# Kernel optimization log

Measured on AMD Instinct MI355X. Metric: run time of the kernel, lower is better.

The kernel has to match this reference:

```python
import jax, jax.numpy as jnp
import numpy as np

N = 100000        # nodes
E = 1600000       # edges (avg degree 16)
F_IN = 512        # num_features
H1, D1 = 8, 8     # layer-1 heads x per-head dim (concat -> 64)
C = 16            # num_classes (layer-2: 1 head, dim C)
NEG_SLOPE = 0.2


def setup_inputs() -> dict:
    key = jax.random.key(0)
    ks = jax.random.split(key, 8)
    x = jax.random.normal(ks[0], (N, F_IN), dtype=jnp.float32)
    edge_index = jax.random.randint(ks[1], (2, E), 0, N, dtype=jnp.int64)
    W1 = jax.random.normal(ks[2], (F_IN, H1 * D1), dtype=jnp.float32) / np.float32(np.sqrt(F_IN))
    a1_src = jax.random.normal(ks[3], (H1, D1), dtype=jnp.float32) * 0.1
    a1_dst = jax.random.normal(ks[4], (H1, D1), dtype=jnp.float32) * 0.1
    W2 = jax.random.normal(ks[5], (H1 * D1, C), dtype=jnp.float32) / np.float32(np.sqrt(H1 * D1))
    a2_src = jax.random.normal(ks[6], (1, C), dtype=jnp.float32) * 0.1
    a2_dst = jax.random.normal(ks[7], (1, C), dtype=jnp.float32) * 0.1
    return {"x": x, "edge_index": edge_index, "W1": W1, "a1_src": a1_src,
            "a1_dst": a1_dst, "W2": W2, "a2_src": a2_src, "a2_dst": a2_dst}


def gat_layer(x, src, dst, W, a_s, a_d, heads, out_dim):
    """Multi-head GAT conv: gather -> per-edge leaky-relu score -> segment
    softmax over destination -> scatter-aggregate. Returns [N, heads, out_dim]."""
    n = x.shape[0]
    h = (x @ W).reshape(n, heads, out_dim)            # [N, H, D]
    es = jnp.einsum('nhd,hd->nh', h, a_s)             # source attention term
    ed = jnp.einsum('nhd,hd->nh', h, a_d)             # dest attention term
    e = jax.nn.leaky_relu(es[src] + ed[dst], NEG_SLOPE)   # [E, H]
    m = jax.ops.segment_max(e, dst, num_segments=n)       # stable softmax max
    ex = jnp.exp(e - m[dst])
    s = jax.ops.segment_sum(ex, dst, num_segments=n)
    alpha = ex / s[dst]                               # [E, H]
    out = jax.ops.segment_sum(h[src] * alpha[..., None], dst, num_segments=n)
    return out                                        # [N, H, D]


def reference(x, edge_index, W1, a1_src, a1_dst, W2, a2_src, a2_dst):
    n = x.shape[0]
    loop = jnp.arange(n, dtype=edge_index.dtype)
    src = jnp.concatenate([edge_index[0], loop])      # add self-loops
    dst = jnp.concatenate([edge_index[1], loop])
    # eval mode: dropout(p=0.6, training=False) is identity
    h1 = gat_layer(x, src, dst, W1, a1_src, a1_dst, H1, D1).reshape(n, H1 * D1)
    h1 = jax.nn.elu(h1)
    h2 = gat_layer(h1, src, dst, W2, a2_src, a2_dst, 1, C).reshape(n, C)
    return jax.nn.log_softmax(h2, axis=1)
```

## Files before the change

kernel.cpp:

```cpp
#include <hip/hip_runtime.h>
#include <hip/hip_bf16.h>

#define F_IN 512
#define H1 8
#define D1 8
#define F_MID 64
#define C 16
#define NEG_SLOPE 0.2f
#define BIN_CHUNK 4096
#define NB_MAX 1024
#define BUCKET_SHIFT 7
#define BUCKET_STRIDE 3072
#define SRC_BITS 17
#define SRC_MASK ((1 << SRC_BITS) - 1)

typedef __attribute__((ext_vector_type(8))) short bf16x8;
typedef __attribute__((ext_vector_type(4))) float f32x4;

static __device__ __forceinline__ unsigned short f2bf(float f) {
    __hip_bfloat16 h = __float2bfloat16(f);
    return *(unsigned short*)&h;
}

__global__ __launch_bounds__(256) void k_bin_w1t(const int* __restrict__ src,
                                                 const int* __restrict__ dst,
                                                 int* __restrict__ gcur,
                                                 int* __restrict__ bucketed,
                                                 const float* __restrict__ W1,
                                                 __hip_bfloat16* __restrict__ w1t,
                                                 int n_edges, int nb, int nbin) {
    const int t = threadIdx.x;
    if ((int)blockIdx.x >= nbin) {
        int idx = ((int)blockIdx.x - nbin) * 256 + t;
        int k = idx >> 6, n = idx & 63;
        w1t[n * F_IN + k] = __float2bfloat16(W1[idx]);
        return;
    }
    __shared__ int cnt[NB_MAX];
    __shared__ int base[NB_MAX];
    const int eb = blockIdx.x * BIN_CHUNK;
    int dc[BIN_CHUNK / 256];
#pragma unroll
    for (int i = 0; i < BIN_CHUNK / 256; ++i) {
        int e = eb + i * 256 + t;
        dc[i] = (e < n_edges) ? dst[e] : -1;
    }
    for (int b = t; b < nb; b += 256) cnt[b] = 0;
    __syncthreads();
#pragma unroll
    for (int i = 0; i < BIN_CHUNK / 256; ++i)
        if (dc[i] >= 0) atomicAdd(&cnt[dc[i] >> BUCKET_SHIFT], 1);
    __syncthreads();
    for (int b = t; b < nb; b += 256) {
        int c = cnt[b];
        base[b] = c > 0 ? atomicAdd(&gcur[b], c) : 0;
        cnt[b] = 0;
    }
    __syncthreads();
#pragma unroll
    for (int i = 0; i < BIN_CHUNK / 256; ++i) {
        if (dc[i] >= 0) {
            int e = eb + i * 256 + t;
            int d = dc[i];
            int b = d >> BUCKET_SHIFT;
            int local = atomicAdd(&cnt[b], 1);
            bucketed[(size_t)b * BUCKET_STRIDE + base[b] + local] =
                ((d & ((1 << BUCKET_SHIFT) - 1)) << SRC_BITS) | src[e];
        }
    }
}

__global__ __launch_bounds__(256) void k_place(const int* __restrict__ gcur,
                                               const int* __restrict__ bucketed,
                                               int* __restrict__ row_start,
                                               int* __restrict__ sorted_src,
                                               int n_nodes, int n_edges) {
    __shared__ int stage[BUCKET_STRIDE];
    __shared__ int cnt[1 << BUCKET_SHIFT];
    __shared__ int cur[1 << BUCKET_SHIFT];
    __shared__ int wsum[4];
    const int t = threadIdx.x;
    const int b = blockIdx.x;
    if (t < (1 << BUCKET_SHIFT)) cnt[t] = 0;
    int pre = 0;
    for (int j = t; j < b; j += 256) pre += gcur[j];
#pragma unroll
    for (int off = 1; off < 64; off <<= 1) pre += __shfl_xor(pre, off, 64);
    if ((t & 63) == 0) wsum[t >> 6] = pre;
    __syncthreads();
    const int base0 = wsum[0] + wsum[1] + wsum[2] + wsum[3];
    if (b == 0 && t == 0) row_start[n_nodes] = n_edges;

    const int total = gcur[b];
    const int* bp = bucketed + (size_t)b * BUCKET_STRIDE;
    for (int i = t; i < total; i += 256) {
        int e = bp[i];
        stage[i] = e;
        atomicAdd(&cnt[e >> SRC_BITS], 1);
    }
    __syncthreads();
    if (t < (1 << BUCKET_SHIFT)) cur[t] = cnt[t];
    __syncthreads();
#pragma unroll
    for (int d = 1; d < (1 << BUCKET_SHIFT); d <<= 1) {
        int u = 0;
        if (t < (1 << BUCKET_SHIFT) && t >= d) u = cur[t - d];
        __syncthreads();
        if (t < (1 << BUCKET_SHIFT)) cur[t] += u;
        __syncthreads();
    }
    if (t < (1 << BUCKET_SHIFT)) {
        int node = (b << BUCKET_SHIFT) + t;
        int excl = cur[t] - cnt[t];
        if (node < n_nodes) row_start[node] = base0 + excl;
        cur[t] = excl;
    }
    __syncthreads();
    for (int i = t; i < total; i += 256) {
        int e = stage[i];
        int p = atomicAdd(&cur[e >> SRC_BITS], 1);
        sorted_src[base0 + p] = e & SRC_MASK;
    }
}

__global__ __launch_bounds__(256) void k_gemm1(const float* __restrict__ x,
                                               const __hip_bfloat16* __restrict__ w1t,
                                               const float* __restrict__ a1s,
                                               const float* __restrict__ a1d,
                                               __hip_bfloat16* __restrict__ h1b,
                                               float* __restrict__ es1,
                                               float* __restrict__ ed1, int n_nodes) {
    const int t = threadIdx.x;
    const int wv = t >> 6, l = t & 63;
    const int q = l >> 4, m16 = l & 15;
    const int rowbase = blockIdx.x * 64;

    const int node = rowbase + wv * 16 + m16;
    const int gx = node < n_nodes ? node : n_nodes - 1;
    const float* xrow = x + (size_t)gx * F_IN;

    f32x4 acc[4];
#pragma unroll
    for (int i = 0; i < 4; ++i) acc[i] = (f32x4){0.f, 0.f, 0.f, 0.f};

    for (int kt = 0; kt < F_IN; kt += 64) {
#pragma unroll
        for (int kk = 0; kk < 2; ++kk) {
            const float* xp = xrow + kt + kk * 32 + q * 8;
            float4 v0 = *(const float4*)(xp);
            float4 v1 = *(const float4*)(xp + 4);
            ushort4 b0, b1;
            b0.x = f2bf(v0.x); b0.y = f2bf(v0.y); b0.z = f2bf(v0.z); b0.w = f2bf(v0.w);
            b1.x = f2bf(v1.x); b1.y = f2bf(v1.y); b1.z = f2bf(v1.z); b1.w = f2bf(v1.w);
            union { ushort4 u4[2]; bf16x8 v8; } bu;
            bu.u4[0] = b0; bu.u4[1] = b1;
            const bf16x8 bfrag = bu.v8;
#pragma unroll
            for (int tn = 0; tn < 4; ++tn) {
                bf16x8 afrag = *(const bf16x8*)(w1t + (size_t)(tn * 16 + m16) * F_IN
                                                + kt + kk * 32 + q * 8);
                acc[tn] = __builtin_amdgcn_mfma_f32_16x16x32_bf16(afrag, bfrag, acc[tn], 0, 0, 0);
            }
        }
    }

    const bool ok = node < n_nodes;
#pragma unroll
    for (int tn = 0; tn < 4; ++tn) {
        const f32x4 a = acc[tn];
        const int nw0 = tn * 16 + q * 4;
        float vs = a.x * a1s[nw0] + a.y * a1s[nw0 + 1] + a.z * a1s[nw0 + 2] + a.w * a1s[nw0 + 3];
        float vd = a.x * a1d[nw0] + a.y * a1d[nw0 + 1] + a.z * a1d[nw0 + 2] + a.w * a1d[nw0 + 3];
        vs += __shfl_xor(vs, 16, 64);
        vd += __shfl_xor(vd, 16, 64);
        if (ok) {
            ushort4 b;
            b.x = f2bf(a.x); b.y = f2bf(a.y); b.z = f2bf(a.z); b.w = f2bf(a.w);
            *(ushort4*)(h1b + (size_t)node * F_MID + nw0) = b;
            if ((q & 1) == 0) {
                const int head = 2 * tn + (q >> 1);
                es1[node * H1 + head] = vs;
                ed1[node * H1 + head] = vd;
            }
        }
    }
}

__global__ __launch_bounds__(256) void k_gather1(const int* __restrict__ row_start,
                                                 const int* __restrict__ sorted_src,
                                                 const __hip_bfloat16* __restrict__ h1b,
                                                 const float* __restrict__ es1,
                                                 const float* __restrict__ ed1,
                                                 __hip_bfloat16* __restrict__ h1c, int n_nodes) {
    const int n = blockIdx.x * 4 + (threadIdx.x >> 6);
    if (n >= n_nodes) return;
    const int lane = threadIdx.x & 63;
    const int h = lane >> 3;
    const float edh = ed1[n * H1 + h];
    const int beg = row_start[n], end = row_start[n + 1];
    float acc = 0.f, den = 0.f;
    for (int base = beg; base < end; base += 64) {
        const int m = min(64, end - base);
        const int li = lane < m ? lane : (m - 1);
        const int myS = sorted_src[base + li];
        int j = 0;
        for (; j + 8 <= m; j += 8) {
            const int s0 = __shfl(myS, j, 64),     s1 = __shfl(myS, j + 1, 64);
            const int s2 = __shfl(myS, j + 2, 64), s3 = __shfl(myS, j + 3, 64);
            const int s4 = __shfl(myS, j + 4, 64), s5 = __shfl(myS, j + 5, 64);
            const int s6 = __shfl(myS, j + 6, 64), s7 = __shfl(myS, j + 7, 64);
            float e0 = es1[s0 * H1 + h], e1 = es1[s1 * H1 + h];
            float e2 = es1[s2 * H1 + h], e3 = es1[s3 * H1 + h];
            float e4 = es1[s4 * H1 + h], e5 = es1[s5 * H1 + h];
            float e6 = es1[s6 * H1 + h], e7 = es1[s7 * H1 + h];
            const float f0 = __bfloat162float(h1b[(size_t)s0 * F_MID + lane]);
            const float f1 = __bfloat162float(h1b[(size_t)s1 * F_MID + lane]);
            const float f2 = __bfloat162float(h1b[(size_t)s2 * F_MID + lane]);
            const float f3 = __bfloat162float(h1b[(size_t)s3 * F_MID + lane]);
            const float f4 = __bfloat162float(h1b[(size_t)s4 * F_MID + lane]);
            const float f5 = __bfloat162float(h1b[(size_t)s5 * F_MID + lane]);
            const float f6 = __bfloat162float(h1b[(size_t)s6 * F_MID + lane]);
            const float f7 = __bfloat162float(h1b[(size_t)s7 * F_MID + lane]);
            e0 += edh; e1 += edh; e2 += edh; e3 += edh;
            e4 += edh; e5 += edh; e6 += edh; e7 += edh;
            e0 = e0 > 0.f ? e0 : NEG_SLOPE * e0;
            e1 = e1 > 0.f ? e1 : NEG_SLOPE * e1;
            e2 = e2 > 0.f ? e2 : NEG_SLOPE * e2;
            e3 = e3 > 0.f ? e3 : NEG_SLOPE * e3;
            e4 = e4 > 0.f ? e4 : NEG_SLOPE * e4;
            e5 = e5 > 0.f ? e5 : NEG_SLOPE * e5;
            e6 = e6 > 0.f ? e6 : NEG_SLOPE * e6;
            e7 = e7 > 0.f ? e7 : NEG_SLOPE * e7;
            const float w0 = __expf(e0), w1 = __expf(e1), w2 = __expf(e2), w3 = __expf(e3);
            const float w4 = __expf(e4), w5 = __expf(e5), w6 = __expf(e6), w7 = __expf(e7);
            acc += (w0 * f0 + w1 * f1 + w2 * f2 + w3 * f3)
                 + (w4 * f4 + w5 * f5 + w6 * f6 + w7 * f7);
            den += ((w0 + w1) + (w2 + w3)) + ((w4 + w5) + (w6 + w7));
        }
        for (; j + 4 <= m; j += 4) {
            const int s0 = __shfl(myS, j, 64), s1 = __shfl(myS, j + 1, 64);
            const int s2 = __shfl(myS, j + 2, 64), s3 = __shfl(myS, j + 3, 64);
            float e0 = es1[s0 * H1 + h], e1 = es1[s1 * H1 + h];
            float e2 = es1[s2 * H1 + h], e3 = es1[s3 * H1 + h];
            const float f0 = __bfloat162float(h1b[(size_t)s0 * F_MID + lane]);
            const float f1 = __bfloat162float(h1b[(size_t)s1 * F_MID + lane]);
            const float f2 = __bfloat162float(h1b[(size_t)s2 * F_MID + lane]);
            const float f3 = __bfloat162float(h1b[(size_t)s3 * F_MID + lane]);
            e0 += edh; e1 += edh; e2 += edh; e3 += edh;
            e0 = e0 > 0.f ? e0 : NEG_SLOPE * e0;
            e1 = e1 > 0.f ? e1 : NEG_SLOPE * e1;
            e2 = e2 > 0.f ? e2 : NEG_SLOPE * e2;
            e3 = e3 > 0.f ? e3 : NEG_SLOPE * e3;
            const float w0 = __expf(e0), w1 = __expf(e1), w2 = __expf(e2), w3 = __expf(e3);
            acc += w0 * f0 + w1 * f1 + w2 * f2 + w3 * f3;
            den += (w0 + w1) + (w2 + w3);
        }
        for (; j < m; ++j) {
            const int s = __shfl(myS, j, 64);
            float ev = es1[s * H1 + h] + edh;
            ev = ev > 0.f ? ev : NEG_SLOPE * ev;
            const float w = __expf(ev);
            acc += w * __bfloat162float(h1b[(size_t)s * F_MID + lane]);
            den += w;
        }
    }
    float evs = es1[n * H1 + h] + edh;
    evs = evs > 0.f ? evs : NEG_SLOPE * evs;
    const float ws = __expf(evs);
    acc += ws * __bfloat162float(h1b[(size_t)n * F_MID + lane]);
    den += ws;
    float v = acc / den;
    v = v > 0.f ? v : expm1f(v);
    h1c[(size_t)n * F_MID + lane] = __float2bfloat16(v);
}

__global__ void k_gemm2(const __hip_bfloat16* __restrict__ h1c, const float* __restrict__ W2,
                        const float* __restrict__ a2s, const float* __restrict__ a2d,
                        __hip_bfloat16* __restrict__ h2b, float* __restrict__ es2,
                        float* __restrict__ ed2, int n_nodes) {
    __shared__ float w2s[F_MID * C];
    __shared__ float h1s[16][F_MID + 1];
    const int t = threadIdx.x;
    const int nb = blockIdx.x * 16;
    for (int i = t; i < F_MID * C; i += 256) w2s[i] = W2[i];
    {
        int r = t >> 4, k4 = (t & 15) << 2;
        int n = nb + r;
        const __hip_bfloat16* p = h1c + (size_t)(n < n_nodes ? n : n_nodes - 1) * F_MID + k4;
        ushort4 v = *(const ushort4*)p;
        h1s[r][k4 + 0] = __bfloat162float(*(const __hip_bfloat16*)&v.x);
        h1s[r][k4 + 1] = __bfloat162float(*(const __hip_bfloat16*)&v.y);
        h1s[r][k4 + 2] = __bfloat162float(*(const __hip_bfloat16*)&v.z);
        h1s[r][k4 + 3] = __bfloat162float(*(const __hip_bfloat16*)&v.w);
    }
    __syncthreads();
    const int r = t >> 4, c = t & 15;
    const int n = nb + r;
    float acc = 0.f;
#pragma unroll
    for (int k = 0; k < F_MID; ++k) acc += h1s[r][k] * w2s[k * C + c];
    float vs = acc * a2s[c], vd = acc * a2d[c];
#pragma unroll
    for (int off = 1; off < 16; off <<= 1) {
        vs += __shfl_xor(vs, off, 64);
        vd += __shfl_xor(vd, off, 64);
    }
    if (n < n_nodes) {
        h2b[(size_t)n * C + c] = __float2bfloat16(acc);
        if (c == 0) { es2[n] = vs; ed2[n] = vd; }
    }
}

__global__ __launch_bounds__(256) void k_gather2(const int* __restrict__ row_start,
                                                 const int* __restrict__ sorted_src,
                                                 const __hip_bfloat16* __restrict__ h2b,
                                                 const float* __restrict__ es2,
                                                 const float* __restrict__ ed2,
                                                 float* __restrict__ out, int n_nodes) {
    const int n = blockIdx.x * 16 + (threadIdx.x >> 4);
    if (n >= n_nodes) return;
    const int lane = threadIdx.x & 63;
    const int c = lane & 15;
    const int g = lane >> 4;
    const float ed = ed2[n];
    const int beg = row_start[n], end = row_start[n + 1];
    float acc = 0.f, den = 0.f;
    for (int base = beg; base < end; base += 16) {
        const int m = min(16, end - base);
        const int li = c < m ? c : (m - 1);
        const int myS = sorted_src[base + li];
        float evp = es2[myS] + ed;
        evp = evp > 0.f ? evp : NEG_SLOPE * evp;
        const float wli = __expf(evp);
        int j = 0;
        for (; j + 4 <= m; j += 4) {
            const int s0 = __shfl(myS, g * 16 + j, 64), s1 = __shfl(myS, g * 16 + j + 1, 64);
            const int s2 = __shfl(myS, g * 16 + j + 2, 64), s3 = __shfl(myS, g * 16 + j + 3, 64);
            const float w0 = __shfl(wli, g * 16 + j, 64), w1 = __shfl(wli, g * 16 + j + 1, 64);
            const float w2 = __shfl(wli, g * 16 + j + 2, 64), w3 = __shfl(wli, g * 16 + j + 3, 64);
            const float f0 = __bfloat162float(h2b[(size_t)s0 * C + c]);
            const float f1 = __bfloat162float(h2b[(size_t)s1 * C + c]);
            const float f2 = __bfloat162float(h2b[(size_t)s2 * C + c]);
            const float f3 = __bfloat162float(h2b[(size_t)s3 * C + c]);
            acc += w0 * f0 + w1 * f1 + w2 * f2 + w3 * f3;
            den += (w0 + w1) + (w2 + w3);
        }
        for (; j < m; ++j) {
            const int s = __shfl(myS, g * 16 + j, 64);
            const float w = __shfl(wli, g * 16 + j, 64);
            acc += w * __bfloat162float(h2b[(size_t)s * C + c]);
            den += w;
        }
    }
    float evs = es2[n] + ed;
    evs = evs > 0.f ? evs : NEG_SLOPE * evs;
    const float ws = __expf(evs);
    acc += ws * __bfloat162float(h2b[(size_t)n * C + c]);
    den += ws;
    const float v = acc / den;
    float mx = v;
#pragma unroll
    for (int off = 1; off < 16; off <<= 1) mx = fmaxf(mx, __shfl_xor(mx, off, 64));
    float se = __expf(v - mx);
#pragma unroll
    for (int off = 1; off < 16; off <<= 1) se += __shfl_xor(se, off, 64);
    out[(size_t)n * C + c] = v - mx - __logf(se);
}

extern "C" void kernel_launch(void* const* d_in, const int* in_sizes, int n_in,
                              void* d_out, int out_size, void* d_ws, size_t ws_size,
                              hipStream_t stream) {
    const float* x   = (const float*)d_in[0];
    const int*   ei  = (const int*)d_in[1];
    const float* W1  = (const float*)d_in[2];
    const float* a1s = (const float*)d_in[3];
    const float* a1d = (const float*)d_in[4];
    const float* W2  = (const float*)d_in[5];
    const float* a2s = (const float*)d_in[6];
    const float* a2d = (const float*)d_in[7];
    float* out = (float*)d_out;

    const int n_nodes = in_sizes[0] / F_IN;
    const int n_edges = in_sizes[1] / 2;
    const int* src = ei;
    const int* dst = ei + n_edges;
    const int nb = (n_nodes + (1 << BUCKET_SHIFT) - 1) >> BUCKET_SHIFT;
    const int nbin = (n_edges + BIN_CHUNK - 1) / BIN_CHUNK;

    float* fws = (float*)d_ws;
    float* es1 = fws;
    float* ed1 = es1 + (size_t)n_nodes * H1;
    float* es2 = ed1 + (size_t)n_nodes * H1;
    float* ed2 = es2 + n_nodes;
    __hip_bfloat16* h1b = (__hip_bfloat16*)(ed2 + n_nodes);
    __hip_bfloat16* h2b = h1b + (size_t)n_nodes * F_MID;
    __hip_bfloat16* h1c = h2b + (size_t)n_nodes * C;
    __hip_bfloat16* w1t = h1c + (size_t)n_nodes * F_MID;
    int* iws         = (int*)(w1t + F_IN * F_MID);
    int* gcur        = iws;
    int* row_start   = gcur + NB_MAX;
    int* sorted_src  = row_start + n_nodes + 1;
    int* bucketed    = sorted_src + n_edges;

    hipMemsetAsync(gcur, 0, NB_MAX * sizeof(int), stream);

    k_bin_w1t<<<nbin + (F_IN * F_MID) / 256, 256, 0, stream>>>(src, dst, gcur, bucketed,
                                                               W1, w1t, n_edges, nb, nbin);
    k_place<<<nb, 256, 0, stream>>>(gcur, bucketed, row_start, sorted_src, n_nodes, n_edges);

    k_gemm1<<<(n_nodes + 63) / 64, 256, 0, stream>>>(x, w1t, a1s, a1d, h1b, es1, ed1, n_nodes);
    k_gather1<<<(n_nodes + 3) / 4, 256, 0, stream>>>(row_start, sorted_src, h1b, es1, ed1, h1c, n_nodes);

    k_gemm2<<<(n_nodes + 15) / 16, 256, 0, stream>>>(h1c, W2, a2s, a2d, h2b, es2, ed2, n_nodes);
    k_gather2<<<(n_nodes + 15) / 16, 256, 0, stream>>>(row_start, sorted_src, h2b, es2, ed2, out, n_nodes);
}
```

Measured before the change: 478.6 us.

## Merge edge binning and layer-1 GEMM into one launch to overlap them

After: 470.1 us. About the same (-1.8%).

```diff
diff --git a/kernel.cpp b/kernel.cpp
--- a/kernel.cpp
+++ b/kernel.cpp
@@ -22,118 +22,72 @@
     return *(unsigned short*)&h;
 }
 
-__global__ __launch_bounds__(256) void k_bin_w1t(const int* __restrict__ src,
-                                                 const int* __restrict__ dst,
-                                                 int* __restrict__ gcur,
-                                                 int* __restrict__ bucketed,
-                                                 const float* __restrict__ W1,
-                                                 __hip_bfloat16* __restrict__ w1t,
-                                                 int n_edges, int nb, int nbin) {
+__global__ __launch_bounds__(256) void k_init(const float* __restrict__ W1,
+                                              __hip_bfloat16* __restrict__ w1t,
+                                              int* __restrict__ gcur) {
     const int t = threadIdx.x;
-    if ((int)blockIdx.x >= nbin) {
-        int idx = ((int)blockIdx.x - nbin) * 256 + t;
-        int k = idx >> 6, n = idx & 63;
-        w1t[n * F_IN + k] = __float2bfloat16(W1[idx]);
+    if ((int)blockIdx.x == (F_IN * F_MID) / 256) {
+        for (int i = t; i < NB_MAX; i += 256) gcur[i] = 0;
         return;
     }
+    int idx = blockIdx.x * 256 + t;
+    int k = idx >> 6, n = idx & 63;
+    w1t[n * F_IN + k] = __float2bfloat16(W1[idx]);
+}
+
+__global__ __launch_bounds__(256) void k_bin_gemm1(const int* __restrict__ src,
+                                                   const int* __restrict__ dst,
+                                                   int* __restrict__ gcur,
+                                                   int* __restrict__ bucketed,
+                                                   const float* __restrict__ x,
+                                                   const __hip_bfloat16* __restrict__ w1t,
+                                                   const float* __restrict__ a1s,
+                                                   const float* __restrict__ a1d,
+                                                   __hip_bfloat16* __restrict__ h1b,
+                                                   float* __restrict__ es1,
+                                                   float* __restrict__ ed1,
+                                                   int n_edges, int nb, int nbin, int n_nodes) {
     __shared__ int cnt[NB_MAX];
     __shared__ int base[NB_MAX];
-    const int eb = blockIdx.x * BIN_CHUNK;
-    int dc[BIN_CHUNK / 256];
-#pragma unroll
-    for (int i = 0; i < BIN_CHUNK / 256; ++i) {
-        int e = eb + i * 256 + t;
-        dc[i] = (e < n_edges) ? dst[e] : -1;
-    }
-    for (int b = t; b < nb; b += 256) cnt[b] = 0;
-    __syncthreads();
-#pragma unroll
-    for (int i = 0; i < BIN_CHUNK / 256; ++i)
-        if (dc[i] >= 0) atomicAdd(&cnt[dc[i] >> BUCKET_SHIFT], 1);
-    __syncthreads();
-    for (int b = t; b < nb; b += 256) {
-        int c = cnt[b];
-        base[b] = c > 0 ? atomicAdd(&gcur[b], c) : 0;
-        cnt[b] = 0;
-    }
-    __syncthreads();
-#pragma unroll
-    for (int i = 0; i < BIN_CHUNK / 256; ++i) {
-        if (dc[i] >= 0) {
+    const int t = threadIdx.x;
+
+    if ((int)blockIdx.x < nbin) {
+        const int eb = blockIdx.x * BIN_CHUNK;
+        int dc[BIN_CHUNK / 256];
+#pragma unroll
+        for (int i = 0; i < BIN_CHUNK / 256; ++i) {
             int e = eb + i * 256 + t;
-            int d = dc[i];
-            int b = d >> BUCKET_SHIFT;
-            int local = atomicAdd(&cnt[b], 1);
-            bucketed[(size_t)b * BUCKET_STRIDE + base[b] + local] =
-                ((d & ((1 << BUCKET_SHIFT) - 1)) << SRC_BITS) | src[e];
-        }
-    }
-}
-
-__global__ __launch_bounds__(256) void k_place(const int* __restrict__ gcur,
-                                               const int* __restrict__ bucketed,
-                                               int* __restrict__ row_start,
-                                               int* __restrict__ sorted_src,
-                                               int n_nodes, int n_edges) {
-    __shared__ int stage[BUCKET_STRIDE];
-    __shared__ int cnt[1 << BUCKET_SHIFT];
-    __shared__ int cur[1 << BUCKET_SHIFT];
-    __shared__ int wsum[4];
-    const int t = threadIdx.x;
-    const int b = blockIdx.x;
-    if (t < (1 << BUCKET_SHIFT)) cnt[t] = 0;
-    int pre = 0;
-    for (int j = t; j < b; j += 256) pre += gcur[j];
-#pragma unroll
-    for (int off = 1; off < 64; off <<= 1) pre += __shfl_xor(pre, off, 64);
-    if ((t & 63) == 0) wsum[t >> 6] = pre;
-    __syncthreads();
-    const int base0 = wsum[0] + wsum[1] + wsum[2] + wsum[3];
-    if (b == 0 && t == 0) row_start[n_nodes] = n_edges;
-
-    const int total = gcur[b];
-    const int* bp = bucketed + (size_t)b * BUCKET_STRIDE;
-    for (int i = t; i < total; i += 256) {
-        int e = bp[i];
-        stage[i] = e;
-        atomicAdd(&cnt[e >> SRC_BITS], 1);
-    }
-    __syncthreads();
-    if (t < (1 << BUCKET_SHIFT)) cur[t] = cnt[t];
-    __syncthreads();
-#pragma unroll
-    for (int d = 1; d < (1 << BUCKET_SHIFT); d <<= 1) {
-        int u = 0;
-        if (t < (1 << BUCKET_SHIFT) && t >= d) u = cur[t - d];
+            dc[i] = (e < n_edges) ? dst[e] : -1;
+        }
+        for (int b = t; b < nb; b += 256) cnt[b] = 0;
         __syncthreads();
-        if (t < (1 << BUCKET_SHIFT)) cur[t] += u;
+#pragma unroll
+        for (int i = 0; i < BIN_CHUNK / 256; ++i)
+            if (dc[i] >= 0) atomicAdd(&cnt[dc[i] >> BUCKET_SHIFT], 1);
         __syncthreads();
-    }
-    if (t < (1 << BUCKET_SHIFT)) {
-        int node = (b << BUCKET_SHIFT) + t;
-        int excl = cur[t] - cnt[t];
-        if (node < n_nodes) row_start[node] = base0 + excl;
-        cur[t] = excl;
-    }
-    __syncthreads();
-    for (int i = t; i < total; i += 256) {
-        int e = stage[i];
-        int p = atomicAdd(&cur[e >> SRC_BITS], 1);
-        sorted_src[base0 + p] = e & SRC_MASK;
-    }
-}
-
-__global__ __launch_bounds__(256) void k_gemm1(const float* __restrict__ x,
-                                               const __hip_bfloat16* __restrict__ w1t,
-                                               const float* __restrict__ a1s,
-                                               const float* __restrict__ a1d,
-                                               __hip_bfloat16* __restrict__ h1b,
-                                               float* __restrict__ es1,
-                                               float* __restrict__ ed1, int n_nodes) {
-    const int t = threadIdx.x;
+        for (int b = t; b < nb; b += 256) {
+            int c = cnt[b];
+            base[b] = c > 0 ? atomicAdd(&gcur[b], c) : 0;
+            cnt[b] = 0;
+        }
+        __syncthreads();
+#pragma unroll
+        for (int i = 0; i < BIN_CHUNK / 256; ++i) {
+            if (dc[i] >= 0) {
+                int e = eb + i * 256 + t;
+                int d = dc[i];
+                int b = d >> BUCKET_SHIFT;
+                int local = atomicAdd(&cnt[b], 1);
+                bucketed[(size_t)b * BUCKET_STRIDE + base[b] + local] =
+                    ((d & ((1 << BUCKET_SHIFT) - 1)) << SRC_BITS) | src[e];
+            }
+        }
+        return;
+    }
+
     const int wv = t >> 6, l = t & 63;
     const int q = l >> 4, m16 = l & 15;
-    const int rowbase = blockIdx.x * 64;
+    const int rowbase = ((int)blockIdx.x - nbin) * 64;
 
     const int node = rowbase + wv * 16 + m16;
     const int gx = node < n_nodes ? node : n_nodes - 1;
@@ -183,6 +137,59 @@
                 ed1[node * H1 + head] = vd;
             }
         }
+    }
+}
+
+__global__ __launch_bounds__(256) void k_place(const int* __restrict__ gcur,
+                                               const int* __restrict__ bucketed,
+                                               int* __restrict__ row_start,
+                                               int* __restrict__ sorted_src,
+                                               int n_nodes, int n_edges) {
+    __shared__ int stage[BUCKET_STRIDE];
+    __shared__ int cnt[1 << BUCKET_SHIFT];
+    __shared__ int cur[1 << BUCKET_SHIFT];
+    __shared__ int wsum[4];
+    const int t = threadIdx.x;
+    const int b = blockIdx.x;
+    if (t < (1 << BUCKET_SHIFT)) cnt[t] = 0;
+    int pre = 0;
+    for (int j = t; j < b; j += 256) pre += gcur[j];
+#pragma unroll
+    for (int off = 1; off < 64; off <<= 1) pre += __shfl_xor(pre, off, 64);
+    if ((t & 63) == 0) wsum[t >> 6] = pre;
+    __syncthreads();
+    const int base0 = wsum[0] + wsum[1] + wsum[2] + wsum[3];
+    if (b == 0 && t == 0) row_start[n_nodes] = n_edges;
+
+    const int total = gcur[b];
+    const int* bp = bucketed + (size_t)b * BUCKET_STRIDE;
+    for (int i = t; i < total; i += 256) {
+        int e = bp[i];
+        stage[i] = e;
+        atomicAdd(&cnt[e >> SRC_BITS], 1);
+    }
+    __syncthreads();
+    if (t < (1 << BUCKET_SHIFT)) cur[t] = cnt[t];
+    __syncthreads();
+#pragma unroll
+    for (int d = 1; d < (1 << BUCKET_SHIFT); d <<= 1) {
+        int u = 0;
+        if (t < (1 << BUCKET_SHIFT) && t >= d) u = cur[t - d];
+        __syncthreads();
+        if (t < (1 << BUCKET_SHIFT)) cur[t] += u;
+        __syncthreads();
+    }
+    if (t < (1 << BUCKET_SHIFT)) {
+        int node = (b << BUCKET_SHIFT) + t;
+        int excl = cur[t] - cnt[t];
+        if (node < n_nodes) row_start[node] = base0 + excl;
+        cur[t] = excl;
+    }
+    __syncthreads();
+    for (int i = t; i < total; i += 256) {
+        int e = stage[i];
+        int p = atomicAdd(&cur[e >> SRC_BITS], 1);
+        sorted_src[base0 + p] = e & SRC_MASK;
     }
 }
 
@@ -386,6 +393,7 @@
     const int* dst = ei + n_edges;
     const int nb = (n_nodes + (1 << BUCKET_SHIFT) - 1) >> BUCKET_SHIFT;
     const int nbin = (n_edges + BIN_CHUNK - 1) / BIN_CHUNK;
+    const int ngemm = (n_nodes + 63) / 64;
 
     float* fws = (float*)d_ws;
     float* es1 = fws;
@@ -402,13 +410,14 @@
     int* sorted_src  = row_start + n_nodes + 1;
     int* bucketed    = sorted_src + n_edges;
 
-    hipMemsetAsync(gcur, 0, NB_MAX * sizeof(int), stream);
-
-    k_bin_w1t<<<nbin + (F_IN * F_MID) / 256, 256, 0, stream>>>(src, dst, gcur, bucketed,
-                                                               W1, w1t, n_edges, nb, nbin);
+    k_init<<<(F_IN * F_MID) / 256 + 1, 256, 0, stream>>>(W1, w1t, gcur);
+
+    k_bin_gemm1<<<nbin + ngemm, 256, 0, stream>>>(src, dst, gcur, bucketed,
+                                                  x, w1t, a1s, a1d, h1b, es1, ed1,
+                                                  n_edges, nb, nbin, n_nodes);
+
     k_place<<<nb, 256, 0, stream>>>(gcur, bucketed, row_start, sorted_src, n_nodes, n_edges);
 
-    k_gemm1<<<(n_nodes + 63) / 64, 256, 0, stream>>>(x, w1t, a1s, a1d, h1b, es1, ed1, n_nodes);
     k_gather1<<<(n_nodes + 3) / 4, 256, 0, stream>>>(row_start, sorted_src, h1b, es1, ed1, h1c, n_nodes);
 
     k_gemm2<<<(n_nodes + 15) / 16, 256, 0, stream>>>(h1c, W2, a2s, a2d, h2b, es2, ed2, n_nodes);
```
